# Kernel optimization log

Hardware: AMD Instinct MI355X
Metric: run time of the kernel (lower is better)

## Reference

```python
import jax, jax.numpy as jnp
import numpy as np

# Grid / problem sizes (match init_kwargs)
B, D, H, W = 2, 64, 256, 256      # batch + spatial_shape
N = 524288                         # active voxels
IN_DIM, HID = 32, 32               # input_dim, hidden_dim
C_IN = IN_DIM + HID                # conv in-channels (64)
C_OUT = 4 * HID                    # conv out-channels (128)
OFFSETS = [(dz, dy, dx) for dz in (-1, 0, 1) for dy in (-1, 0, 1) for dx in (-1, 0, 1)]


def setup_inputs() -> dict:
    key = jax.random.key(0)
    ks = jax.random.split(key, 5)
    # Unique active-voxel coordinates: odd multiplier is a bijection mod 2^k grid size.
    total = B * D * H * W
    MULT = 2654435761  # odd => injective on arange(N) mod total (total is a power of 2)
    lin = (np.arange(N, dtype=np.int64) * MULT) % total
    b = lin // (D * H * W)
    r = lin % (D * H * W)
    z = r // (H * W)
    r = r % (H * W)
    y = r // W
    x = r % W
    coors = jnp.asarray(np.stack([b, z, y, x], axis=1).astype(np.int32))  # [N,4]
    x_features = jax.random.normal(ks[0], (N, IN_DIM), jnp.float32)
    h_features = jax.random.normal(ks[1], (N, HID), jnp.float32)
    c_features = jax.random.normal(ks[2], (N, HID), jnp.float32)
    weight = jax.random.normal(ks[3], (27, C_IN, C_OUT), jnp.float32) * 0.05
    bias = jax.random.normal(ks[4], (C_OUT,), jnp.float32) * 0.05
    return {"x_features": x_features, "h_features": h_features,
            "c_features": c_features, "weight": weight, "bias": bias,
            "coors": coors, "batch_size": B}


def _subm_conv3d(feats, weight, bias, coors):
    """Submanifold sparse 3x3x3 conv: output only at active sites;
    gather-GEMM-scatter via a dense coordinate->point-id map (the rulebook)."""
    b, z, y, x = coors[:, 0], coors[:, 1], coors[:, 2], coors[:, 3]
    pid = jnp.arange(N, dtype=jnp.int32)
    idx_map = jnp.full((B, D, H, W), -1, jnp.int32).at[b, z, y, x].set(pid)
    out = jnp.zeros((N, C_OUT), feats.dtype) + bias  # [N, 4*HID]
    for k, (dz, dy, dx) in enumerate(OFFSETS):
        nz, ny, nx = z + dz, y + dy, x + dx
        inb = (nz >= 0) & (nz < D) & (ny >= 0) & (ny < H) & (nx >= 0) & (nx < W)
        nid = idx_map[b, jnp.clip(nz, 0, D - 1), jnp.clip(ny, 0, H - 1), jnp.clip(nx, 0, W - 1)]
        nid = jnp.where(inb, nid, -1)
        valid = nid >= 0
        gathered = jnp.where(valid[:, None], feats[jnp.maximum(nid, 0)], 0.0)  # [N, C_IN]
        out = out + gathered @ weight[k]
    return out


def reference(x_features, h_features, c_features, weight, bias, coors, batch_size):
    combined = jnp.concatenate([x_features, h_features], axis=1)  # [N, C_IN]
    cc = _subm_conv3d(combined, weight, bias, coors)              # [N, 4*HID]
    cc_i, cc_f, cc_o, cc_g = jnp.split(cc, 4, axis=1)
    i = jax.nn.sigmoid(cc_i)
    f = jax.nn.sigmoid(cc_f)
    o = jax.nn.sigmoid(cc_o)
    g = jnp.tanh(cc_g)
    c_next = f * c_features + i * g
    h_next = o * jnp.tanh(c_next)
    return (h_next, c_next)
```

## Files before the change

kernel.cpp:

```cpp
#include <hip/hip_runtime.h>
#include <stdint.h>

#define N_PTS 524288
#define DQ 64
#define HQ 256
#define WQ 256
#define MAP_BYTES (2*DQ*HQ*WQ*4)

typedef short bf8  __attribute__((ext_vector_type(8)));
typedef float f16v __attribute__((ext_vector_type(16)));

static __device__ __forceinline__ short f2bf(float f) {
    union { float f; uint32_t u; } v; v.f = f;
    return (short)((v.u + 0x7fffu + ((v.u >> 16) & 1u)) >> 16);
}
static __device__ __forceinline__ float fast_sigmoid(float x) {
    return 1.f / (1.f + __expf(-x));
}
static __device__ __forceinline__ float fast_tanh(float x) {
    return 1.f - 2.f / (__expf(2.f * x) + 1.f);
}

__global__ void k_feats(const float* __restrict__ xf, const float* __restrict__ hf,
                        const int* __restrict__ coors, short* __restrict__ fb,
                        int* __restrict__ map) {
    int t = blockIdx.x * 256 + threadIdx.x;
    int n = t >> 3, seg = t & 7;
    const float* src = (seg < 4) ? (xf + n*32 + seg*8) : (hf + n*32 + seg*8 - 32);
    float4 a = ((const float4*)src)[0];
    float4 b = ((const float4*)src)[1];
    bf8 r;
    r[0]=f2bf(a.x); r[1]=f2bf(a.y); r[2]=f2bf(a.z); r[3]=f2bf(a.w);
    r[4]=f2bf(b.x); r[5]=f2bf(b.y); r[6]=f2bf(b.z); r[7]=f2bf(b.w);
    ((bf8*)fb)[t] = r;
    if (seg == 0) {
        int4 c = ((const int4*)coors)[n];
        map[((c.x*DQ + c.y)*HQ + c.z)*WQ + c.w] = n;
    }
}

__global__ void k_wt(const float* __restrict__ w, short* __restrict__ wt) {
    int t = blockIdx.x * 256 + threadIdx.x;
    if (t >= 27*64*128) return;
    int jj = t & 7, c = (t >> 3) & 127, jg = (t >> 10) & 7, k = t >> 13;
    int j = jg*8 + jj;
    wt[t] = f2bf(w[(k*64 + j)*128 + c]);
}

__launch_bounds__(256, 2)
__global__ void k_main(const int* __restrict__ map, const short* __restrict__ fb,
                       const short* __restrict__ wt, const float* __restrict__ bias,
                       const float* __restrict__ cfeat, const int* __restrict__ coors,
                       const short* __restrict__ zp, float* __restrict__ out)
{
    __shared__ short Wlds[2][8192];

    const int tid  = threadIdx.x;
    const int lane = tid & 63;
    const int wv   = tid >> 6;
    const int l31  = lane & 31;
    const int lhi  = lane >> 5;

    const int pbase = blockIdx.x * 256;
    const int p     = pbase + wv*64 + lane;

    const int4 cr = ((const int4*)coors)[p];
    const int mbase = ((cr.x*DQ + cr.y)*HQ + cr.z)*WQ + cr.w;

    auto probe = [&](int ko) -> int {
        int dz = ko/9 - 1, dy = (ko/3)%3 - 1, dxo = ko%3 - 1;
        if ((unsigned)(cr.y + dz) < (unsigned)DQ &&
            (unsigned)(cr.z + dy) < (unsigned)HQ &&
            (unsigned)(cr.w + dxo) < (unsigned)WQ)
            return map[mbase + (dz*HQ + dy)*WQ + dxo];
        return -1;
    };

    auto stageW = [&](int ko) {
        const short* src = wt + ko*8192;
        #pragma unroll
        for (int i = 0; i < 4; i++) {
            int cb = i*256 + wv*64;
            __builtin_amdgcn_global_load_lds(
                (const __attribute__((address_space(1))) void*)(src + (size_t)(cb + lane)*8),
                (__attribute__((address_space(3))) void*)&Wlds[ko & 1][cb*8],
                16, 0, 0);
        }
    };

    auto gather = [&](int n0, int n1, bf8* dst) {
        const short* s0 = (n0 >= 0) ? (fb + (size_t)n0*64 + lhi*8) : (zp + lhi*8);
        const short* s1 = (n1 >= 0) ? (fb + (size_t)n1*64 + lhi*8) : (zp + lhi*8);
        #pragma unroll
        for (int j = 0; j < 4; j++) {
            dst[j]     = *(const bf8*)(s0 + j*16);
            dst[4 + j] = *(const bf8*)(s1 + j*16);
        }
    };

    f16v acc[2][4];
    #pragma unroll
    for (int mt = 0; mt < 2; mt++)
        #pragma unroll
        for (int ct = 0; ct < 4; ct++) {
            float bv = bias[ct*32 + l31];
            #pragma unroll
            for (int r = 0; r < 16; r++) acc[mt][ct][r] = bv;
        }

    int pA = probe(0);
    int pB = probe(1);
    int pr_old = probe(2);
    stageW(0);

    bf8 a_cur[8], a_next[8];
    {
        int g0 = __shfl(pA, l31, 64);
        int g1 = __shfl(pA, l31 + 32, 64);
        gather(g0, g1, a_cur);
    }
    int g0n = __shfl(pB, l31, 64);
    int g1n = __shfl(pB, l31 + 32, 64);

    #pragma unroll 1
    for (int ko = 0; ko < 27; ko++) {
        __syncthreads();

        if (ko < 26) {
            stageW(ko + 1);
            gather(g0n, g1n, a_next);
        }
        int pr_new = (ko < 24) ? probe(ko + 3) : -1;

        const int buf = ko & 1;
        #pragma unroll
        for (int ks = 0; ks < 4; ks++) {
            int jg = ks*2 + lhi;
            const short* wb = &Wlds[buf][(jg*128 + l31)*8];
            #pragma unroll
            for (int ct = 0; ct < 4; ct++) {
                bf8 b = *(const bf8*)(wb + ct*32*8);
                acc[0][ct] = __builtin_amdgcn_mfma_f32_32x32x16_bf16(a_cur[ks],     b, acc[0][ct], 0, 0, 0);
                acc[1][ct] = __builtin_amdgcn_mfma_f32_32x32x16_bf16(a_cur[4 + ks], b, acc[1][ct], 0, 0, 0);
            }
        }

        if (ko < 25) {
            g0n = __shfl(pr_old, l31, 64);
            g1n = __shfl(pr_old, l31 + 32, 64);
            pr_old = pr_new;
        }
        #pragma unroll
        for (int j = 0; j < 8; j++) a_cur[j] = a_next[j];
    }

    #pragma unroll
    for (int mt = 0; mt < 2; mt++) {
        #pragma unroll
        for (int r = 0; r < 16; r++) {
            int row = (r & 3) + 8*(r >> 2) + 4*lhi;
            int pp  = pbase + wv*64 + mt*32 + row;
            float gi = acc[mt][0][r];
            float gf = acc[mt][1][r];
            float go = acc[mt][2][r];
            float gg = acc[mt][3][r];
            float cv = cfeat[pp*32 + l31];
            float si = fast_sigmoid(gi);
            float sf = fast_sigmoid(gf);
            float so = fast_sigmoid(go);
            float tg = fast_tanh(gg);
            float cn = sf*cv + si*tg;
            float hn = so * fast_tanh(cn);
            out[pp*32 + l31] = hn;
            out[N_PTS*32 + pp*32 + l31] = cn;
        }
    }
}

extern "C" void kernel_launch(void* const* d_in, const int* in_sizes, int n_in,
                              void* d_out, int out_size, void* d_ws, size_t ws_size,
                              hipStream_t stream) {
    const float* xf    = (const float*)d_in[0];
    const float* hf    = (const float*)d_in[1];
    const float* cf    = (const float*)d_in[2];
    const float* w     = (const float*)d_in[3];
    const float* bias  = (const float*)d_in[4];
    const int*   coors = (const int*)d_in[5];
    float* out = (float*)d_out;

    int*   map = (int*)d_ws;
    short* fb  = (short*)((char*)d_ws + MAP_BYTES);
    short* wtb = (short*)((char*)d_ws + MAP_BYTES + (size_t)N_PTS*64*2);
    short* zp  = (short*)((char*)d_ws + MAP_BYTES + (size_t)N_PTS*64*2 + 27*64*128*2);

    hipMemsetAsync(map, 0xFF, MAP_BYTES, stream);
    hipMemsetAsync(zp, 0, 256, stream);
    k_feats<<<(N_PTS*8)/256, 256, 0, stream>>>(xf, hf, coors, fb, map);
    k_wt<<<(27*64*128 + 255)/256, 256, 0, stream>>>(w, wtb);
    k_main<<<N_PTS/256, 256, 0, stream>>>(map, fb, wtb, bias, cf, coors, zp, out);
}
```

Measured before the change: 501.2 us.

## Spatially sort active voxels via bucket counting sort to improve gather locality

Adds a histogram, scan and rank pass that buckets voxels by coarse linear grid position. Features, coordinates and the map are stored in that sorted order, so neighbour gathers in the main kernel hit nearby rows of the feature buffer and the map. Block indices are also swizzled across eight groups, and outputs are scattered back to the original order through a permutation array. This adds three small kernels, atomics and scattered cfeat reads and output writes.

```diff
diff --git a/kernel.cpp b/kernel.cpp
--- a/kernel.cpp
+++ b/kernel.cpp
@@ -6,6 +6,7 @@
 #define HQ 256
 #define WQ 256
 #define MAP_BYTES (2*DQ*HQ*WQ*4)
+#define NBKT 4096
 
 typedef short bf8  __attribute__((ext_vector_type(8)));
 typedef float f16v __attribute__((ext_vector_type(16)));
@@ -21,21 +22,64 @@
     return 1.f - 2.f / (__expf(2.f * x) + 1.f);
 }
 
+__global__ void k_hist(const int* __restrict__ coors, int* __restrict__ hist) {
+    int n = blockIdx.x * 256 + threadIdx.x;
+    int4 c = ((const int4*)coors)[n];
+    int mbase = ((c.x*DQ + c.y)*HQ + c.z)*WQ + c.w;
+    atomicAdd(&hist[mbase >> 11], 1);
+}
+
+__global__ void k_scan(int* __restrict__ hist) {
+    __shared__ int wsum[4];
+    int tid = threadIdx.x;
+    int lane = tid & 63, wv = tid >> 6;
+    int v[16]; int s = 0;
+    #pragma unroll
+    for (int i = 0; i < 16; i++) { v[i] = hist[tid*16 + i]; s += v[i]; }
+    int sc = s;
+    #pragma unroll
+    for (int d = 1; d < 64; d <<= 1) {
+        int t = __shfl_up(sc, d, 64);
+        if (lane >= d) sc += t;
+    }
+    if (lane == 63) wsum[wv] = sc;
+    __syncthreads();
+    int base = 0;
+    #pragma unroll
+    for (int w = 0; w < 4; w++) if (w < wv) base += wsum[w];
+    int excl = base + sc - s;
+    #pragma unroll
+    for (int i = 0; i < 16; i++) { int c = v[i]; hist[tid*16 + i] = excl; excl += c; }
+}
+
+__global__ void k_rank(const int* __restrict__ coors, int* __restrict__ hist,
+                       int* __restrict__ rank, int* __restrict__ sorg) {
+    int n = blockIdx.x * 256 + threadIdx.x;
+    int4 c = ((const int4*)coors)[n];
+    int mbase = ((c.x*DQ + c.y)*HQ + c.z)*WQ + c.w;
+    int slot = atomicAdd(&hist[mbase >> 11], 1);
+    rank[n] = slot;
+    sorg[slot] = n;
+}
+
 __global__ void k_feats(const float* __restrict__ xf, const float* __restrict__ hf,
-                        const int* __restrict__ coors, short* __restrict__ fb,
-                        int* __restrict__ map) {
+                        const int* __restrict__ coors, const int* __restrict__ rank,
+                        short* __restrict__ fb, int* __restrict__ map,
+                        int4* __restrict__ rcoors) {
     int t = blockIdx.x * 256 + threadIdx.x;
     int n = t >> 3, seg = t & 7;
+    int r = rank[n];
     const float* src = (seg < 4) ? (xf + n*32 + seg*8) : (hf + n*32 + seg*8 - 32);
     float4 a = ((const float4*)src)[0];
     float4 b = ((const float4*)src)[1];
-    bf8 r;
-    r[0]=f2bf(a.x); r[1]=f2bf(a.y); r[2]=f2bf(a.z); r[3]=f2bf(a.w);
-    r[4]=f2bf(b.x); r[5]=f2bf(b.y); r[6]=f2bf(b.z); r[7]=f2bf(b.w);
-    ((bf8*)fb)[t] = r;
+    bf8 rv;
+    rv[0]=f2bf(a.x); rv[1]=f2bf(a.y); rv[2]=f2bf(a.z); rv[3]=f2bf(a.w);
+    rv[4]=f2bf(b.x); rv[5]=f2bf(b.y); rv[6]=f2bf(b.z); rv[7]=f2bf(b.w);
+    ((bf8*)fb)[r*8 + seg] = rv;
     if (seg == 0) {
         int4 c = ((const int4*)coors)[n];
-        map[((c.x*DQ + c.y)*HQ + c.z)*WQ + c.w] = n;
+        map[((c.x*DQ + c.y)*HQ + c.z)*WQ + c.w] = r;
+        rcoors[r] = c;
     }
 }
 
@@ -50,8 +94,9 @@
 __launch_bounds__(256, 2)
 __global__ void k_main(const int* __restrict__ map, const short* __restrict__ fb,
                        const short* __restrict__ wt, const float* __restrict__ bias,
-                       const float* __restrict__ cfeat, const int* __restrict__ coors,
-                       const short* __restrict__ zp, float* __restrict__ out)
+                       const float* __restrict__ cfeat, const int4* __restrict__ rcoors,
+                       const int* __restrict__ sorg, const short* __restrict__ zp,
+                       float* __restrict__ out)
 {
     __shared__ short Wlds[2][8192];
 
@@ -61,10 +106,11 @@
     const int l31  = lane & 31;
     const int lhi  = lane >> 5;
 
-    const int pbase = blockIdx.x * 256;
+    const int bid   = (blockIdx.x & 7) * 256 + (blockIdx.x >> 3);
+    const int pbase = bid * 256;
     const int p     = pbase + wv*64 + lane;
 
-    const int4 cr = ((const int4*)coors)[p];
+    const int4 cr = rcoors[p];
     const int mbase = ((cr.x*DQ + cr.y)*HQ + cr.z)*WQ + cr.w;
 
     auto probe = [&](int ko) -> int {
@@ -160,19 +206,20 @@
         for (int r = 0; r < 16; r++) {
             int row = (r & 3) + 8*(r >> 2) + 4*lhi;
             int pp  = pbase + wv*64 + mt*32 + row;
+            int orig = sorg[pp];
             float gi = acc[mt][0][r];
             float gf = acc[mt][1][r];
             float go = acc[mt][2][r];
             float gg = acc[mt][3][r];
-            float cv = cfeat[pp*32 + l31];
+            float cv = cfeat[orig*32 + l31];
             float si = fast_sigmoid(gi);
             float sf = fast_sigmoid(gf);
             float so = fast_sigmoid(go);
             float tg = fast_tanh(gg);
             float cn = sf*cv + si*tg;
             float hn = so * fast_tanh(cn);
-            out[pp*32 + l31] = hn;
-            out[N_PTS*32 + pp*32 + l31] = cn;
+            out[orig*32 + l31] = hn;
+            out[N_PTS*32 + orig*32 + l31] = cn;
         }
     }
 }
@@ -188,14 +235,23 @@
     const int*   coors = (const int*)d_in[5];
     float* out = (float*)d_out;
 
-    int*   map = (int*)d_ws;
-    short* fb  = (short*)((char*)d_ws + MAP_BYTES);
-    short* wtb = (short*)((char*)d_ws + MAP_BYTES + (size_t)N_PTS*64*2);
-    short* zp  = (short*)((char*)d_ws + MAP_BYTES + (size_t)N_PTS*64*2 + 27*64*128*2);
+    char* base = (char*)d_ws;
+    int*   map    = (int*)base;
+    short* fb     = (short*)(base + MAP_BYTES);
+    short* wtb    = (short*)(base + MAP_BYTES + (size_t)N_PTS*64*2);
+    short* zp     = (short*)(base + 100663296 + 442368);
+    int*   rank   = (int*)(base + 101106176);
+    int*   sorg   = (int*)(base + 103203328);
+    int4*  rcoors = (int4*)(base + 105300480);
+    int*   hist   = (int*)(base + 113689088);
 
     hipMemsetAsync(map, 0xFF, MAP_BYTES, stream);
+    hipMemsetAsync(hist, 0, NBKT*4, stream);
     hipMemsetAsync(zp, 0, 256, stream);
-    k_feats<<<(N_PTS*8)/256, 256, 0, stream>>>(xf, hf, coors, fb, map);
+    k_hist<<<N_PTS/256, 256, 0, stream>>>(coors, hist);
+    k_scan<<<1, 256, 0, stream>>>(hist);
+    k_rank<<<N_PTS/256, 256, 0, stream>>>(coors, hist, rank, sorg);
+    k_feats<<<(N_PTS*8)/256, 256, 0, stream>>>(xf, hf, coors, rank, fb, map, rcoors);
     k_wt<<<(27*64*128 + 255)/256, 256, 0, stream>>>(w, wtb);
-    k_main<<<N_PTS/256, 256, 0, stream>>>(map, fb, wtb, bias, cf, coors, zp, out);
-}
+    k_main<<<N_PTS/256, 256, 0, stream>>>(map, fb, wtb, bias, cf, rcoors, sorg, zp, out);
+}
```

Measured after the change: 581.1 us. 15.9% more time.

## Fuse prep kernels and hand-schedule main loop with partial vmcnt waits

Applied to the files above, without the earlier changes.

Merges the feature/map and weight conversion kernels into one launch that also zeroes the pad buffer, removing a memset and a launch. The neighbor probe becomes branchless with clamped map loads. The main loop is unrolled by two so the double-buffered A fragments swap without register copies, and __syncthreads is replaced by explicit s_waitcnt vmcnt(N) plus s_barrier so that gather and probe loads can stay in flight across the barrier. The hand-tuned waitcnt values depend on the exact issued load counts and could be fragile.

```diff
diff --git a/kernel.cpp b/kernel.cpp
--- a/kernel.cpp
+++ b/kernel.cpp
@@ -6,6 +6,8 @@
 #define HQ 256
 #define WQ 256
 #define MAP_BYTES (2*DQ*HQ*WQ*4)
+#define FEAT_BLOCKS ((N_PTS*8)/256)
+#define WT_BLOCKS   ((27*64*128 + 255)/256)
 
 typedef short bf8  __attribute__((ext_vector_type(8)));
 typedef float f16v __attribute__((ext_vector_type(16)));
@@ -21,30 +23,35 @@
     return 1.f - 2.f / (__expf(2.f * x) + 1.f);
 }
 
-__global__ void k_feats(const float* __restrict__ xf, const float* __restrict__ hf,
-                        const int* __restrict__ coors, short* __restrict__ fb,
-                        int* __restrict__ map) {
-    int t = blockIdx.x * 256 + threadIdx.x;
-    int n = t >> 3, seg = t & 7;
-    const float* src = (seg < 4) ? (xf + n*32 + seg*8) : (hf + n*32 + seg*8 - 32);
-    float4 a = ((const float4*)src)[0];
-    float4 b = ((const float4*)src)[1];
-    bf8 r;
-    r[0]=f2bf(a.x); r[1]=f2bf(a.y); r[2]=f2bf(a.z); r[3]=f2bf(a.w);
-    r[4]=f2bf(b.x); r[5]=f2bf(b.y); r[6]=f2bf(b.z); r[7]=f2bf(b.w);
-    ((bf8*)fb)[t] = r;
-    if (seg == 0) {
-        int4 c = ((const int4*)coors)[n];
-        map[((c.x*DQ + c.y)*HQ + c.z)*WQ + c.w] = n;
-    }
-}
-
-__global__ void k_wt(const float* __restrict__ w, short* __restrict__ wt) {
-    int t = blockIdx.x * 256 + threadIdx.x;
-    if (t >= 27*64*128) return;
-    int jj = t & 7, c = (t >> 3) & 127, jg = (t >> 10) & 7, k = t >> 13;
-    int j = jg*8 + jj;
-    wt[t] = f2bf(w[(k*64 + j)*128 + c]);
+__global__ void k_prep(const float* __restrict__ xf, const float* __restrict__ hf,
+                       const int* __restrict__ coors, const float* __restrict__ w,
+                       short* __restrict__ fb, int* __restrict__ map,
+                       short* __restrict__ wt, short* __restrict__ zp) {
+    int b = blockIdx.x;
+    if (b < FEAT_BLOCKS) {
+        int t = b * 256 + threadIdx.x;
+        int n = t >> 3, seg = t & 7;
+        const float* src = (seg < 4) ? (xf + n*32 + seg*8) : (hf + n*32 + seg*8 - 32);
+        float4 a = ((const float4*)src)[0];
+        float4 bb = ((const float4*)src)[1];
+        bf8 rv;
+        rv[0]=f2bf(a.x); rv[1]=f2bf(a.y); rv[2]=f2bf(a.z); rv[3]=f2bf(a.w);
+        rv[4]=f2bf(bb.x); rv[5]=f2bf(bb.y); rv[6]=f2bf(bb.z); rv[7]=f2bf(bb.w);
+        ((bf8*)fb)[t] = rv;
+        if (seg == 0) {
+            int4 c = ((const int4*)coors)[n];
+            map[((c.x*DQ + c.y)*HQ + c.z)*WQ + c.w] = n;
+        }
+    } else {
+        int t = (b - FEAT_BLOCKS) * 256 + threadIdx.x;
+        if (t < 27*64*128) {
+            int jj = t & 7, c = (t >> 3) & 127, jg = (t >> 10) & 7, k = t >> 13;
+            int j = jg*8 + jj;
+            wt[t] = f2bf(w[(k*64 + j)*128 + c]);
+        }
+        if (b == FEAT_BLOCKS + WT_BLOCKS - 1 && threadIdx.x < 32)
+            ((int4*)zp)[threadIdx.x] = int4{0,0,0,0};
+    }
 }
 
 __launch_bounds__(256, 2)
@@ -65,15 +72,18 @@
     const int p     = pbase + wv*64 + lane;
 
     const int4 cr = ((const int4*)coors)[p];
-    const int mbase = ((cr.x*DQ + cr.y)*HQ + cr.z)*WQ + cr.w;
+    const int mb0 = cr.x*DQ;
 
     auto probe = [&](int ko) -> int {
         int dz = ko/9 - 1, dy = (ko/3)%3 - 1, dxo = ko%3 - 1;
-        if ((unsigned)(cr.y + dz) < (unsigned)DQ &&
-            (unsigned)(cr.z + dy) < (unsigned)HQ &&
-            (unsigned)(cr.w + dxo) < (unsigned)WQ)
-            return map[mbase + (dz*HQ + dy)*WQ + dxo];
-        return -1;
+        int nz = cr.y + dz, ny = cr.z + dy, nx = cr.w + dxo;
+        bool inb = ((unsigned)nz < (unsigned)DQ) & ((unsigned)ny < (unsigned)HQ) &
+                   ((unsigned)nx < (unsigned)WQ);
+        int cz = min(max(nz, 0), DQ-1);
+        int cy = min(max(ny, 0), HQ-1);
+        int cx = min(max(nx, 0), WQ-1);
+        int nid = map[((mb0 + cz)*HQ + cy)*WQ + cx];
+        return inb ? nid : -1;
     };
 
     auto stageW = [&](int ko) {
@@ -108,51 +118,69 @@
             for (int r = 0; r < 16; r++) acc[mt][ct][r] = bv;
         }
 
+    stageW(0);
     int pA = probe(0);
     int pB = probe(1);
     int pr_old = probe(2);
-    stageW(0);
-
-    bf8 a_cur[8], a_next[8];
+
+    bf8 fA[8], fB[8];
     {
         int g0 = __shfl(pA, l31, 64);
         int g1 = __shfl(pA, l31 + 32, 64);
-        gather(g0, g1, a_cur);
+        gather(g0, g1, fA);
     }
     int g0n = __shfl(pB, l31, 64);
     int g1n = __shfl(pB, l31 + 32, 64);
 
+    __builtin_amdgcn_sched_barrier(0);
+    asm volatile("s_waitcnt vmcnt(0)" ::: "memory");
+    __builtin_amdgcn_s_barrier();
+    __builtin_amdgcn_sched_barrier(0);
+
+#define ITER_BODY(KO, FA, FB)                                                     \
+    {                                                                             \
+        const int _ko = (KO);                                                     \
+        if (_ko < 26) {                                                           \
+            stageW(_ko + 1);                        \
+            __builtin_amdgcn_sched_barrier(0);                                    \
+            gather(g0n, g1n, FB);                 \
+            __builtin_amdgcn_sched_barrier(0);                                    \
+        }                                                                         \
+        int pr_new = (_ko < 24) ? probe(_ko + 3) : -1;                \
+        const int buf = _ko & 1;                                                  \
+        _Pragma("unroll")                                                         \
+        for (int ks = 0; ks < 4; ks++) {                                          \
+            int jg = ks*2 + lhi;                                                  \
+            const short* wb = &Wlds[buf][(jg*128 + l31)*8];                       \
+            _Pragma("unroll")                                                     \
+            for (int ct = 0; ct < 4; ct++) {                                      \
+                bf8 b = *(const bf8*)(wb + ct*32*8);                              \
+                acc[0][ct] = __builtin_amdgcn_mfma_f32_32x32x16_bf16(FA[ks],     b, acc[0][ct], 0, 0, 0); \
+                acc[1][ct] = __builtin_amdgcn_mfma_f32_32x32x16_bf16(FA[4 + ks], b, acc[1][ct], 0, 0, 0); \
+            }                                                                     \
+        }                                                                         \
+        if (_ko < 25) {                                 \
+            g0n = __shfl(pr_old, l31, 64);                                        \
+            g1n = __shfl(pr_old, l31 + 32, 64);                                   \
+            pr_old = pr_new;                                                      \
+        }                                                                         \
+        if (_ko < 26) {                                                           \
+            __builtin_amdgcn_sched_barrier(0);                                    \
+            \
+            if (_ko < 24) { asm volatile("s_waitcnt vmcnt(9)" ::: "memory"); }    \
+            else          { asm volatile("s_waitcnt vmcnt(8)" ::: "memory"); }    \
+            __builtin_amdgcn_s_barrier();                                         \
+            __builtin_amdgcn_sched_barrier(0);                                    \
+        }                                                                         \
+    }
+
     #pragma unroll 1
-    for (int ko = 0; ko < 27; ko++) {
-        __syncthreads();
-
-        if (ko < 26) {
-            stageW(ko + 1);
-            gather(g0n, g1n, a_next);
-        }
-        int pr_new = (ko < 24) ? probe(ko + 3) : -1;
-
-        const int buf = ko & 1;
-        #pragma unroll
-        for (int ks = 0; ks < 4; ks++) {
-            int jg = ks*2 + lhi;
-            const short* wb = &Wlds[buf][(jg*128 + l31)*8];
-            #pragma unroll
-            for (int ct = 0; ct < 4; ct++) {
-                bf8 b = *(const bf8*)(wb + ct*32*8);
-                acc[0][ct] = __builtin_amdgcn_mfma_f32_32x32x16_bf16(a_cur[ks],     b, acc[0][ct], 0, 0, 0);
-                acc[1][ct] = __builtin_amdgcn_mfma_f32_32x32x16_bf16(a_cur[4 + ks], b, acc[1][ct], 0, 0, 0);
-            }
-        }
-
-        if (ko < 25) {
-            g0n = __shfl(pr_old, l31, 64);
-            g1n = __shfl(pr_old, l31 + 32, 64);
-            pr_old = pr_new;
-        }
-        #pragma unroll
-        for (int j = 0; j < 8; j++) a_cur[j] = a_next[j];
-    }
+    for (int ko = 0; ko < 26; ko += 2) {
+        ITER_BODY(ko,     fA, fB)
+        ITER_BODY(ko + 1, fB, fA)
+    }
+    ITER_BODY(26, fA, fB)
+#undef ITER_BODY
 
     #pragma unroll
     for (int mt = 0; mt < 2; mt++) {
@@ -188,14 +216,13 @@
     const int*   coors = (const int*)d_in[5];
     float* out = (float*)d_out;
 
-    int*   map = (int*)d_ws;
-    short* fb  = (short*)((char*)d_ws + MAP_BYTES);
-    short* wtb = (short*)((char*)d_ws + MAP_BYTES + (size_t)N_PTS*64*2);
-    short* zp  = (short*)((char*)d_ws + MAP_BYTES + (size_t)N_PTS*64*2 + 27*64*128*2);
+    char* base = (char*)d_ws;
+    int*   map    = (int*)base;
+    short* fb     = (short*)(base + MAP_BYTES);
+    short* wtb    = (short*)(base + 100663296);
+    short* zp     = (short*)(base + 101105664);
 
     hipMemsetAsync(map, 0xFF, MAP_BYTES, stream);
-    hipMemsetAsync(zp, 0, 256, stream);
-    k_feats<<<(N_PTS*8)/256, 256, 0, stream>>>(xf, hf, coors, fb, map);
-    k_wt<<<(27*64*128 + 255)/256, 256, 0, stream>>>(w, wtb);
+    k_prep<<<FEAT_BLOCKS + WT_BLOCKS, 256, 0, stream>>>(xf, hf, coors, w, fb, map, wtb, zp);
     k_main<<<N_PTS/256, 256, 0, stream>>>(map, fb, wtb, bias, cf, coors, zp, out);
 }
```

New measurement: 524.1 us. +4.6%, slower.
